# Kernel tuning notes

Hardware: AMD Instinct MI355X
Metric: run time of the kernel (lower is better)

## Reference

```python
import jax, jax.numpy as jnp
import numpy as np

N_MOLS, N_CONFS_PER, A = 64, 10, 40
N_CONFS = N_MOLS * N_CONFS_PER   # 640
N_ATOMS = N_CONFS * A            # 25600
N_EDGES = 409600
D, F, NG, L = 256, 256, 32, 4    # n_atom_basis, n_filters, n_gaussians, n_convolutions
MOL_BASIS = 512
CUTOFF = 5.0
LOG2 = float(np.log(2.0))


def ssp(x):
    # shifted softplus, the SchNet nonlinearity
    return jax.nn.softplus(x) - LOG2


def setup_inputs() -> dict:
    key = jax.random.key(0)
    ks = jax.random.split(key, 20)
    z = jax.random.randint(ks[0], (N_ATOMS,), 1, 100)          # atomic numbers (0 is padding)
    xyz = jax.random.normal(ks[1], (N_ATOMS, 3)) * 2.0
    # neighbor list: pairs of atoms within the same conformer block
    conf = jax.random.randint(ks[2], (N_EDGES,), 0, N_CONFS)
    i = conf * A + jax.random.randint(ks[3], (N_EDGES,), 0, A)
    j = conf * A + jax.random.randint(ks[4], (N_EDGES,), 0, A)
    nbr_list = jnp.stack([i, j], axis=1)
    # statistical boltzmann weights, normalized within each molecule
    w = jax.random.uniform(ks[5], (N_MOLS, N_CONFS_PER))
    boltz_weights = (w / w.sum(axis=1, keepdims=True)).reshape(-1)

    def glorot(k, shape):
        fan = shape[-2] + shape[-1]
        return jax.random.normal(k, shape) * np.sqrt(2.0 / fan)

    emb = (jax.random.normal(ks[6], (100, D)) * 0.1).at[0].set(0.0)  # padding_idx=0
    H = (D + MOL_BASIS) // 2  # 384
    params = dict(
        We1=glorot(ks[7], (L, NG, NG)), be1=jnp.zeros((L, NG)),
        We2=glorot(ks[8], (L, NG, F)),  be2=jnp.zeros((L, F)),
        Wn=glorot(ks[9], (L, D, F)),    bn=jnp.zeros((L, F)),
        Wu1=glorot(ks[10], (L, F, D)),  bu1=jnp.zeros((L, D)),
        Wu2=glorot(ks[11], (L, D, D)),  bu2=jnp.zeros((L, D)),
        Wm1=glorot(ks[12], (D, H)),            bm1=jnp.zeros((H,)),
        Wm2=glorot(ks[13], (H, MOL_BASIS)),    bm2=jnp.zeros((MOL_BASIS,)),
        Wr1=glorot(ks[14], (MOL_BASIS, MOL_BASIS // 2)), br1=jnp.zeros((MOL_BASIS // 2,)),
        Wr2=glorot(ks[15], (MOL_BASIS // 2, 1)),         br2=jnp.zeros((1,)),
    )
    return dict(z=z, xyz=xyz, nbr_list=nbr_list, boltz_weights=boltz_weights, emb=emb, **params)


def reference(z, xyz, nbr_list, boltz_weights, emb,
              We1, be1, We2, be2, Wn, bn, Wu1, bu1, Wu2, bu2,
              Wm1, bm1, Wm2, bm2, Wr1, br1, Wr2, br2):
    a0, a1 = nbr_list[:, 0], nbr_list[:, 1]
    # pair distances -> gaussian smearing (fixed, non-trainable) [E, NG]
    d = jnp.sqrt(jnp.sum((xyz[a0] - xyz[a1]) ** 2, axis=1))
    offsets = jnp.linspace(0.0, CUTOFF, NG)
    width = offsets[1] - offsets[0]
    e_g = jnp.exp(-0.5 * ((d[:, None] - offsets[None, :]) / width) ** 2)

    r = emb[z]  # [N, D] atom embeddings
    for l in range(L):
        # edge filter network: Dense -> ssp -> Dense,  [E, F]
        ef = ssp(e_g @ We1[l] + be1[l]) @ We2[l] + be2[l]
        # node filter [N, F]
        rn = r @ Wn[l] + bn[l]
        # symmetric gather-multiply-scatter (undirected neighbor list)
        agg = jax.ops.segment_sum(rn[a1] * ef, a0, num_segments=N_ATOMS)
        agg = agg + jax.ops.segment_sum(rn[a0] * ef, a1, num_segments=N_ATOMS)
        # update network with residual
        r = r + (ssp(agg @ Wu1[l] + bu1[l]) @ Wu2[l] + bu2[l])

    # sum-pool atoms into conformer fingerprints [C, D]
    conf_fp = r.reshape(N_CONFS, A, D).sum(axis=1)
    # mol_fp_nn -> [C, MOL_BASIS]
    mol_conf_fp = ssp(conf_fp @ Wm1 + bm1) @ Wm2 + bm2
    # boltzmann 'multiply': weight each conformer fp and sum per molecule
    mol_fp = (mol_conf_fp * boltz_weights[:, None]).reshape(N_MOLS, N_CONFS_PER, MOL_BASIS).sum(axis=1)
    # readout head (classifier -> sigmoid)
    out = jax.nn.sigmoid(ssp(mol_fp @ Wr1 + br1) @ Wr2 + br2)  # [N_MOLS, 1]
    return out
```

## Files before the change

kernel.cpp:

```cpp
#include <hip/hip_runtime.h>
#include <hip/hip_bf16.h>

#define N_MOLS      64
#define N_CONFS_PER 10
#define A_ATOMS     40
#define N_CONFS     640
#define N_ATOMS     25600
#define N_EDGES     409600
#define D           256
#define NG          32
#define NLAYERS     4
#define MOLB        512
#define H_MOL       384
#define EDGE_CAP    1024
#define EB          32
#define NBMAX       32
#define SHBP        36
#define SEFP        260
#define SBH         256
#define TPB         512

typedef __attribute__((ext_vector_type(8))) short bshort8;
typedef __attribute__((ext_vector_type(4))) float f32x4;

#define SWZ(row, hw) (((row) << 8) + ((hw) ^ (((row) & 7) << 3)))

__device__ __forceinline__ float sspf(float x) {
    return fmaxf(x, 0.f) + __logf(1.f + __expf(-fabsf(x))) - 0.69314718055994531f;
}
__device__ __forceinline__ float b2f(short s) {
    union { unsigned u; float f; } u;
    u.u = ((unsigned)(unsigned short)s) << 16;
    return u.f;
}
__device__ __forceinline__ short f2bf(float x) {
    return (short)(unsigned short)((__float_as_uint(x) + 0x8000u) >> 16);
}
__device__ __forceinline__ unsigned pkbf(float lo_e, float hi_e) {
    return __builtin_amdgcn_perm(__float_as_uint(hi_e) + 0x8000u,
                                 __float_as_uint(lo_e) + 0x8000u, 0x07060302u);
}

__global__ __launch_bounds__(256) void k_prep(const float* __restrict__ Wn,
                                              const float* __restrict__ Wu1,
                                              const float* __restrict__ Wu2,
                                              __hip_bfloat16* __restrict__ WT) {
    int idx = blockIdx.x * 256 + threadIdx.x;
    int k = idx & 255;
    int n = (idx >> 8) & 255;
    int l = (idx >> 16) & 3;
    int mat = idx >> 18;
    const float* src = (mat == 0) ? Wn : (mat == 1) ? Wu1 : Wu2;
    WT[idx] = __float2bfloat16(src[((size_t)l * 256 + k) * 256 + n]);
}

__global__ __launch_bounds__(256) void k_prep2(const float* __restrict__ We2,
                                               const float* __restrict__ We1,
                                               __hip_bfloat16* __restrict__ WT2,
                                               __hip_bfloat16* __restrict__ We1T) {
    int idx = blockIdx.x * 256 + threadIdx.x;
    if (idx < 32768) {
        int k = idx & 31;
        int n = (idx >> 5) & 255;
        int l = idx >> 13;
        WT2[idx] = __float2bfloat16(We2[((size_t)l * 32 + k) * 256 + n]);
    } else {
        int j = idx - 32768;
        int m = j & 31;
        int t = (j >> 5) & 31;
        int l = j >> 10;
        We1T[j] = __float2bfloat16(We1[((size_t)l * 32 + m) * 32 + t]);
    }
}

__global__ __launch_bounds__(256) void k_scatter(const int* __restrict__ nbr,
                                                 unsigned* __restrict__ cursors,
                                                 unsigned* __restrict__ esort) {
    int e = blockIdx.x * 256 + threadIdx.x;
    if (e >= N_EDGES) return;
    int a0 = nbr[2 * e], a1 = nbr[2 * e + 1];
    int conf = a0 / A_ATOMS;
    int a0l = a0 - conf * A_ATOMS;
    int a1l = a1 - conf * A_ATOMS;
    unsigned r = atomicAdd(&cursors[conf], 1u);
    if (r < EDGE_CAP) esort[conf * EDGE_CAP + r] = (unsigned)((a0l << 6) | a1l);
}

__device__ __forceinline__ void mfma_dense8b(const short* __restrict__ src,
                                             const __hip_bfloat16* __restrict__ WT,
                                             f32x4 acc[3][2], int lane, int wv) {
    const int r = lane & 15, g = lane >> 4;
#pragma unroll
    for (int mt = 0; mt < 3; ++mt)
#pragma unroll
        for (int j = 0; j < 2; ++j) acc[mt][j] = (f32x4){0.f, 0.f, 0.f, 0.f};
#pragma unroll 2
    for (int kt = 0; kt < 8; ++kt) {
        const int ko = kt * 32 + g * 8;
        bshort8 a0 = *(const bshort8*)&src[SWZ(0 * 16 + r, ko)];
        bshort8 a1 = *(const bshort8*)&src[SWZ(1 * 16 + r, ko)];
        bshort8 a2 = *(const bshort8*)&src[SWZ(2 * 16 + r, ko)];
#pragma unroll
        for (int j = 0; j < 2; ++j) {
            const int nt = wv * 2 + j;
            bshort8 b = *(const bshort8*)&WT[(nt * 16 + r) * 256 + ko];
            acc[0][j] = __builtin_amdgcn_mfma_f32_16x16x32_bf16(a0, b, acc[0][j], 0, 0, 0);
            acc[1][j] = __builtin_amdgcn_mfma_f32_16x16x32_bf16(a1, b, acc[1][j], 0, 0, 0);
            acc[2][j] = __builtin_amdgcn_mfma_f32_16x16x32_bf16(a2, b, acc[2][j], 0, 0, 0);
        }
    }
}

template <int MODE>
__device__ __forceinline__ void mfma_wb8b(const f32x4 acc[3][2], short* __restrict__ dst16,
                                          const float* __restrict__ bias, int lane, int wv) {
    const int cc = lane & 15, g = lane >> 4;
    const int cr = g * 4;
#pragma unroll
    for (int j = 0; j < 2; ++j) {
        const int col = (wv * 2 + j) * 16 + cc;
        const float bv = bias[col];
#pragma unroll
        for (int mt = 0; mt < 3; ++mt) {
            if (mt == 2 && g >= 2) continue;
#pragma unroll
            for (int reg = 0; reg < 4; ++reg) {
                const int row = mt * 16 + cr + reg;
                float v = acc[mt][j][reg] + bv;
                if (MODE == 1) v = sspf(v);
                dst16[SWZ(row, col)] = f2bf(v);
            }
        }
    }
}

__global__ __launch_bounds__(TPB, 4) void k_main(
    const int* __restrict__ z, const float* __restrict__ xyz,
    const float* __restrict__ emb,
    const float* __restrict__ be1, const float* __restrict__ be2,
    const float* __restrict__ bn,
    const float* __restrict__ bu1, const float* __restrict__ bu2,
    const __hip_bfloat16* __restrict__ WT,
    const __hip_bfloat16* __restrict__ WT2,
    const __hip_bfloat16* __restrict__ We1T,
    const unsigned* __restrict__ cursors, const unsigned* __restrict__ esort,
    float* __restrict__ conf_fp)
{
    __shared__ short sRb[48 * SBH];
    __shared__ short sBb[48 * SBH];
    __shared__ __align__(16) char uEFbuf[EB * SEFP * 2];
    __shared__ __align__(16) char sHbBuf[2 * EB * SHBP * 2];
    __shared__ float sDall[EDGE_CAP];
    __shared__ unsigned short sCsr[2 * EDGE_CAP];
    __shared__ unsigned short sWin[A_ATOMS * (NBMAX + 1)];
    __shared__ int sPtr[A_ATOMS + 1];

    short* sEFs = (short*)uEFbuf;
    float* colsum = (float*)uEFbuf;
    float (*sXYZ)[3] = (float(*)[3])uEFbuf;
    int* sZ   = (int*)(uEFbuf + 480);
    int* sDeg = (int*)(uEFbuf + 640);
    short (*sHb)[EB * SHBP] = (short(*)[EB * SHBP])sHbBuf;
    unsigned* sEdge = (unsigned*)sHbBuf;

    const int tid  = threadIdx.x;
    const int lane = tid & 63;
    const int wv   = tid >> 6;
    const int c4   = lane << 2;
    const int conf = blockIdx.x;
    const int fr = lane & 15, fg = lane >> 4, g8 = (lane >> 4) << 3;
    const int mtx = wv & 1;
    const int ttx = (wv >> 1) & 1;

    if (tid < A_ATOMS) {
        int ga = conf * A_ATOMS + tid;
        sZ[tid] = z[ga];
        sXYZ[tid][0] = xyz[ga * 3 + 0];
        sXYZ[tid][1] = xyz[ga * 3 + 1];
        sXYZ[tid][2] = xyz[ga * 3 + 2];
        sDeg[tid] = 0;
    }
    for (int i = tid; i < 8 * SBH; i += TPB) {
        sRb[40 * SBH + i] = 0;
        sBb[40 * SBH + i] = 0;
    }
    __syncthreads();
    float embsum = 0.f;
    {
        const int c = tid & 255, q = tid >> 8;
        for (int aa = q; aa < A_ATOMS; aa += 2) {
            float v = emb[sZ[aa] * D + c];
            embsum += v;
            sRb[SWZ(aa, c)] = f2bf(v);
        }
    }
    int cnt = (int)cursors[conf];
    if (cnt > EDGE_CAP) cnt = EDGE_CAP;
    const unsigned* eptr = esort + conf * EDGE_CAP;
    for (int i = tid; i < cnt; i += TPB) {
        unsigned pe = eptr[i];
        sEdge[i] = pe;
        int a0l = (pe >> 6) & 63, a1l = pe & 63;
        float dx = sXYZ[a0l][0] - sXYZ[a1l][0];
        float dy = sXYZ[a0l][1] - sXYZ[a1l][1];
        float dz = sXYZ[a0l][2] - sXYZ[a1l][2];
        sDall[i] = sqrtf(dx * dx + dy * dy + dz * dz) * (31.0f / 5.0f);
        atomicAdd(&sDeg[a0l], 1);
        atomicAdd(&sDeg[a1l], 1);
    }
    for (int i = cnt + tid; i < EDGE_CAP; i += TPB) sDall[i] = 0.f;
    __syncthreads();
    if (tid == 0) {
        int s = 0;
        for (int a = 0; a < A_ATOMS; ++a) { sPtr[a] = s; s += sDeg[a]; }
        sPtr[A_ATOMS] = s;
    }
    __syncthreads();
    const int NB = (cnt + EB - 1) / EB;
    if (tid < A_ATOMS) {
        const int ps = sPtr[tid];
        int pos = ps;
        for (int i = 0; i < cnt; ++i) {
            unsigned pe = sEdge[i];
            int a0l = (pe >> 6) & 63, a1l = pe & 63;
            if (a0l == tid) sCsr[pos++] = (unsigned short)((a1l << 10) | i);
            if (a1l == tid) sCsr[pos++] = (unsigned short)((a0l << 10) | i);
        }
        int p = ps;
        for (int b = 0; b <= NB; ++b) {
            const int lim = b * EB;
            while (p < pos && (int)(sCsr[p] & 1023) < lim) ++p;
            sWin[tid * (NBMAX + 1) + b] = (unsigned short)p;
        }
    }

    float csum[2] = {0.f, 0.f};

    for (int l = 0; l < NLAYERS; ++l) {
        __syncthreads();
        {
            f32x4 acc[3][2];
            mfma_dense8b(sRb, WT + ((size_t)(0 * 4 + l) << 16), acc, lane, wv);
            mfma_wb8b<0>(acc, sBb, bn + l * D, lane, wv);
        }
        __syncthreads();
        float4 agg[5];
#pragma unroll
        for (int k = 0; k < 5; ++k) agg[k] = make_float4(0.f, 0.f, 0.f, 0.f);
        {
            const bshort8 bf0 = *(const bshort8*)&WT2[(size_t)l * 8192 + ((2 * wv + 0) * 16 + fr) * 32 + g8];
            const bshort8 bf1 = *(const bshort8*)&WT2[(size_t)l * 8192 + ((2 * wv + 1) * 16 + fr) * 32 + g8];
            const float bb0 = be2[l * D + (2 * wv + 0) * 16 + fr];
            const float bb1 = be2[l * D + (2 * wv + 1) * 16 + fr];
            const bshort8 bfX = *(const bshort8*)&We1T[(size_t)l * 1024 + (ttx * 16 + fr) * 32 + g8];
            const float bbX = be1[l * NG + ttx * 16 + fr];

            if (wv < 4 && NB > 0) {
                const float dd = sDall[mtx * 16 + fr];
                union { bshort8 v; unsigned u[4]; } ua;
#pragma unroll
                for (int j = 0; j < 4; ++j) {
                    const float u0 = dd - (float)(g8 + 2 * j + 0);
                    const float u1 = dd - (float)(g8 + 2 * j + 1);
                    ua.u[j] = pkbf(__expf(-0.5f * u0 * u0), __expf(-0.5f * u1 * u1));
                }
                f32x4 c = (f32x4){0.f, 0.f, 0.f, 0.f};
                c = __builtin_amdgcn_mfma_f32_16x16x32_bf16(ua.v, bfX, c, 0, 0, 0);
#pragma unroll
                for (int reg = 0; reg < 4; ++reg) {
                    const int erow = mtx * 16 + fg * 4 + reg;
                    sHb[0][erow * SHBP + ttx * 16 + fr] = f2bf(sspf(c[reg] + bbX));
                }
            }
            __syncthreads();
            for (int b = 0; b < NB; ++b) {
                const int base = b * EB;
                {
                    const short* __restrict__ hb = sHb[b & 1];
#pragma unroll
                    for (int mt = 0; mt < 2; ++mt) {
                        union { bshort8 v; short4 s[2]; } af;
                        af.s[0] = *(const short4*)&hb[(mt * 16 + fr) * SHBP + g8];
                        af.s[1] = *(const short4*)&hb[(mt * 16 + fr) * SHBP + g8 + 4];
                        f32x4 c0 = (f32x4){0.f, 0.f, 0.f, 0.f};
                        c0 = __builtin_amdgcn_mfma_f32_16x16x32_bf16(af.v, bf0, c0, 0, 0, 0);
                        f32x4 c1 = (f32x4){0.f, 0.f, 0.f, 0.f};
                        c1 = __builtin_amdgcn_mfma_f32_16x16x32_bf16(af.v, bf1, c1, 0, 0, 0);
#pragma unroll
                        for (int reg = 0; reg < 4; ++reg) {
                            const int erow = mt * 16 + fg * 4 + reg;
                            sEFs[erow * SEFP + (2 * wv + 0) * 16 + fr] = f2bf(c0[reg] + bb0);
                            sEFs[erow * SEFP + (2 * wv + 1) * 16 + fr] = f2bf(c1[reg] + bb1);
                        }
                    }
                }
                if (wv < 4 && b + 1 < NB) {
                    short* __restrict__ hb = sHb[(b + 1) & 1];
                    const float dd = sDall[(b + 1) * EB + mtx * 16 + fr];
                    union { bshort8 v; unsigned u[4]; } ua;
#pragma unroll
                    for (int j = 0; j < 4; ++j) {
                        const float u0 = dd - (float)(g8 + 2 * j + 0);
                        const float u1 = dd - (float)(g8 + 2 * j + 1);
                        ua.u[j] = pkbf(__expf(-0.5f * u0 * u0), __expf(-0.5f * u1 * u1));
                    }
                    f32x4 c = (f32x4){0.f, 0.f, 0.f, 0.f};
                    c = __builtin_amdgcn_mfma_f32_16x16x32_bf16(ua.v, bfX, c, 0, 0, 0);
#pragma unroll
                    for (int reg = 0; reg < 4; ++reg) {
                        const int erow = mtx * 16 + fg * 4 + reg;
                        hb[erow * SHBP + ttx * 16 + fr] = f2bf(sspf(c[reg] + bbX));
                    }
                }
                __syncthreads();
#pragma unroll
                for (int k = 0; k < 5; ++k) {
                    const int row = wv * 5 + k;
                    const int st = (int)sWin[row * (NBMAX + 1) + b];
                    const int en = (int)sWin[row * (NBMAX + 1) + b + 1];
                    for (int i = st; i < en; ++i) {
                        const int ent = (int)sCsr[i];
                        const int e = ent & 1023, src = ent >> 10;
                        const short4 f4 = *(const short4*)&sEFs[(e - base) * SEFP + c4];
                        const short4 r4 = *(const short4*)&sBb[SWZ(src, c4)];
                        agg[k].x = fmaf(b2f(f4.x), b2f(r4.x), agg[k].x);
                        agg[k].y = fmaf(b2f(f4.y), b2f(r4.y), agg[k].y);
                        agg[k].z = fmaf(b2f(f4.z), b2f(r4.z), agg[k].z);
                        agg[k].w = fmaf(b2f(f4.w), b2f(r4.w), agg[k].w);
                    }
                }
                __syncthreads();
            }
        }
#pragma unroll
        for (int k = 0; k < 5; ++k) {
            uint2 p;
            p.x = pkbf(agg[k].x, agg[k].y);
            p.y = pkbf(agg[k].z, agg[k].w);
            *(uint2*)&sBb[SWZ(wv * 5 + k, c4)] = p;
        }
        __syncthreads();
        {
            f32x4 acc[3][2];
            mfma_dense8b(sBb, WT + ((size_t)(1 * 4 + l) << 16), acc, lane, wv);
            __syncthreads();
            mfma_wb8b<1>(acc, sBb, bu1 + l * D, lane, wv);
        }
        __syncthreads();
        {
            f32x4 acc[3][2];
            mfma_dense8b(sBb, WT + ((size_t)(2 * 4 + l) << 16), acc, lane, wv);
            const int cc = lane & 15, g = lane >> 4, cr = g * 4;
#pragma unroll
            for (int j = 0; j < 2; ++j) {
                const int col = (wv * 2 + j) * 16 + cc;
                const float bv = bu2[l * D + col];
#pragma unroll
                for (int mt = 0; mt < 3; ++mt) {
                    if (mt == 2 && g >= 2) continue;
#pragma unroll
                    for (int reg = 0; reg < 4; ++reg) {
                        const int row = mt * 16 + cr + reg;
                        float v = acc[mt][j][reg] + bv;
                        csum[j] += v;
                        const int idx = SWZ(row, col);
                        sRb[idx] = f2bf(b2f(sRb[idx]) + v);
                    }
                }
            }
        }
    }
    __syncthreads();
    if (tid < D) colsum[tid] = 0.f;
    __syncthreads();
    {
        const int cc = lane & 15;
#pragma unroll
        for (int j = 0; j < 2; ++j)
            atomicAdd(&colsum[(wv * 2 + j) * 16 + cc], csum[j]);
        atomicAdd(&colsum[tid & 255], embsum);
    }
    __syncthreads();
    if (tid < D) conf_fp[conf * D + tid] = colsum[tid];
}

__global__ __launch_bounds__(512) void k_mol(
    const float* __restrict__ conf_fp,
    const float* __restrict__ Wm1, const float* __restrict__ bm1,
    const float* __restrict__ Wm2, const float* __restrict__ bm2,
    const float* __restrict__ boltz, float* __restrict__ mol_fp)
{
    __shared__ float cf[D];
    __shared__ float t[H_MOL];
    const int conf = blockIdx.x;
    const int tid = threadIdx.x;
    if (tid < D) cf[tid] = conf_fp[conf * D + tid];
    __syncthreads();
    if (tid < H_MOL) {
        float s = bm1[tid];
        for (int k = 0; k < D; k += 4) {
            const float4 v = *(const float4*)&cf[k];
            s = fmaf(v.x, Wm1[(k + 0) * H_MOL + tid], s);
            s = fmaf(v.y, Wm1[(k + 1) * H_MOL + tid], s);
            s = fmaf(v.z, Wm1[(k + 2) * H_MOL + tid], s);
            s = fmaf(v.w, Wm1[(k + 3) * H_MOL + tid], s);
        }
        t[tid] = sspf(s);
    }
    __syncthreads();
    {
        const int m = tid;
        float s = bm2[m];
        for (int h = 0; h < H_MOL; h += 4) {
            const float4 v = *(const float4*)&t[h];
            s = fmaf(v.x, Wm2[(h + 0) * MOLB + m], s);
            s = fmaf(v.y, Wm2[(h + 1) * MOLB + m], s);
            s = fmaf(v.z, Wm2[(h + 2) * MOLB + m], s);
            s = fmaf(v.w, Wm2[(h + 3) * MOLB + m], s);
        }
        atomicAdd(&mol_fp[(conf / N_CONFS_PER) * MOLB + m], s * boltz[conf]);
    }
}

__global__ __launch_bounds__(256) void k_final(
    const float* __restrict__ mol_fp,
    const float* __restrict__ Wr1, const float* __restrict__ br1,
    const float* __restrict__ Wr2, const float* __restrict__ br2,
    float* __restrict__ out)
{
    __shared__ float mf[MOLB];
    __shared__ float t2[D];
    __shared__ float red[4];
    const int mol = blockIdx.x, tid = threadIdx.x;
    mf[tid]       = mol_fp[mol * MOLB + tid];
    mf[tid + 256] = mol_fp[mol * MOLB + tid + 256];
    __syncthreads();
    {
        float s = br1[tid];
        for (int k = 0; k < MOLB; k += 4) {
            const float4 v = *(const float4*)&mf[k];
            s = fmaf(v.x, Wr1[(k + 0) * D + tid], s);
            s = fmaf(v.y, Wr1[(k + 1) * D + tid], s);
            s = fmaf(v.z, Wr1[(k + 2) * D + tid], s);
            s = fmaf(v.w, Wr1[(k + 3) * D + tid], s);
        }
        t2[tid] = sspf(s);
    }
    __syncthreads();
    float p = t2[tid] * Wr2[tid];
#pragma unroll
    for (int o = 32; o > 0; o >>= 1) p += __shfl_down(p, o);
    if ((tid & 63) == 0) red[tid >> 6] = p;
    __syncthreads();
    if (tid == 0) {
        float logit = red[0] + red[1] + red[2] + red[3] + br2[0];
        out[mol] = 1.f / (1.f + expf(-logit));
    }
}

extern "C" void kernel_launch(void* const* d_in, const int* in_sizes, int n_in,
                              void* d_out, int out_size, void* d_ws, size_t ws_size,
                              hipStream_t stream)
{
    const int*   z     = (const int*)d_in[0];
    const float* xyz   = (const float*)d_in[1];
    const int*   nbr   = (const int*)d_in[2];
    const float* boltz = (const float*)d_in[3];
    const float* emb   = (const float*)d_in[4];
    const float* We1   = (const float*)d_in[5];
    const float* be1   = (const float*)d_in[6];
    const float* We2   = (const float*)d_in[7];
    const float* be2   = (const float*)d_in[8];
    const float* Wn    = (const float*)d_in[9];
    const float* bn    = (const float*)d_in[10];
    const float* Wu1   = (const float*)d_in[11];
    const float* bu1   = (const float*)d_in[12];
    const float* Wu2   = (const float*)d_in[13];
    const float* bu2   = (const float*)d_in[14];
    const float* Wm1   = (const float*)d_in[15];
    const float* bm1   = (const float*)d_in[16];
    const float* Wm2   = (const float*)d_in[17];
    const float* bm2   = (const float*)d_in[18];
    const float* Wr1   = (const float*)d_in[19];
    const float* br1   = (const float*)d_in[20];
    const float* Wr2   = (const float*)d_in[21];
    const float* br2   = (const float*)d_in[22];

    char* ws = (char*)d_ws;
    unsigned* cursors        = (unsigned*)ws;
    float*    mol_fp         = (float*)(ws + 2560);
    unsigned* esort          = (unsigned*)(ws + 133632);
    float*    conf_fp        = (float*)(ws + 2755072);
    __hip_bfloat16* WT       = (__hip_bfloat16*)(ws + 3410432);
    __hip_bfloat16* WT2      = (__hip_bfloat16*)(ws + 4983296);
    __hip_bfloat16* We1T     = (__hip_bfloat16*)(ws + 5048832);

    hipMemsetAsync(cursors, 0, 2560 + 131072, stream);
    k_prep<<<3072, 256, 0, stream>>>(Wn, Wu1, Wu2, WT);
    k_prep2<<<144, 256, 0, stream>>>(We2, We1, WT2, We1T);
    k_scatter<<<(N_EDGES + 255) / 256, 256, 0, stream>>>(nbr, cursors, esort);
    k_main<<<N_CONFS, TPB, 0, stream>>>(z, xyz, emb, be1, be2, bn,
                                        bu1, bu2, WT, WT2, We1T, cursors, esort, conf_fp);
    k_mol<<<N_CONFS, 512, 0, stream>>>(conf_fp, Wm1, bm1, Wm2, bm2, boltz, mol_fp);
    k_final<<<N_MOLS, 256, 0, stream>>>(mol_fp, Wr1, br1, Wr2, br2, (float*)d_out);
}
```

Baseline: 855.8 us.

## Merge prep kernels into one launch and fuse mol MLP into main kernel

Combines the three preprocessing kernels (weight transposes and edge bucketing) into a single launch partitioned by block index, and folds the per-conformer molecular MLP and Boltzmann-weighted accumulation into the tail of the main kernel, reading the conformer fingerprint straight from shared memory. This removes two kernel launches and the conf_fp round trip through global memory. In exchange the main kernel carries extra code and register pressure in its epilogue, which could hurt occupancy. The 384-float MLP scratch now shares the edge-filter buffer.

```diff
diff --git a/kernel.cpp b/kernel.cpp
--- a/kernel.cpp
+++ b/kernel.cpp
@@ -41,49 +41,50 @@
                                  __float_as_uint(lo_e) + 0x8000u, 0x07060302u);
 }
 
-__global__ __launch_bounds__(256) void k_prep(const float* __restrict__ Wn,
-                                              const float* __restrict__ Wu1,
-                                              const float* __restrict__ Wu2,
-                                              __hip_bfloat16* __restrict__ WT) {
-    int idx = blockIdx.x * 256 + threadIdx.x;
-    int k = idx & 255;
-    int n = (idx >> 8) & 255;
-    int l = (idx >> 16) & 3;
-    int mat = idx >> 18;
-    const float* src = (mat == 0) ? Wn : (mat == 1) ? Wu1 : Wu2;
-    WT[idx] = __float2bfloat16(src[((size_t)l * 256 + k) * 256 + n]);
-}
-
-__global__ __launch_bounds__(256) void k_prep2(const float* __restrict__ We2,
-                                               const float* __restrict__ We1,
-                                               __hip_bfloat16* __restrict__ WT2,
-                                               __hip_bfloat16* __restrict__ We1T) {
-    int idx = blockIdx.x * 256 + threadIdx.x;
-    if (idx < 32768) {
-        int k = idx & 31;
-        int n = (idx >> 5) & 255;
-        int l = idx >> 13;
-        WT2[idx] = __float2bfloat16(We2[((size_t)l * 32 + k) * 256 + n]);
+#define PREP_WT_BLOCKS   3072
+#define PREP_W2_BLOCKS   144
+#define PREP_SC_BLOCKS   1600
+__global__ __launch_bounds__(256) void k_prep_all(
+    const float* __restrict__ Wn, const float* __restrict__ Wu1,
+    const float* __restrict__ Wu2, const float* __restrict__ We2,
+    const float* __restrict__ We1, const int* __restrict__ nbr,
+    __hip_bfloat16* __restrict__ WT, __hip_bfloat16* __restrict__ WT2,
+    __hip_bfloat16* __restrict__ We1T,
+    unsigned* __restrict__ cursors, unsigned* __restrict__ esort)
+{
+    const int bid = blockIdx.x;
+    if (bid < PREP_WT_BLOCKS) {
+        int idx = bid * 256 + threadIdx.x;
+        int k = idx & 255;
+        int n = (idx >> 8) & 255;
+        int l = (idx >> 16) & 3;
+        int mat = idx >> 18;
+        const float* src = (mat == 0) ? Wn : (mat == 1) ? Wu1 : Wu2;
+        WT[idx] = __float2bfloat16(src[((size_t)l * 256 + k) * 256 + n]);
+    } else if (bid < PREP_WT_BLOCKS + PREP_W2_BLOCKS) {
+        int idx = (bid - PREP_WT_BLOCKS) * 256 + threadIdx.x;
+        if (idx < 32768) {
+            int k = idx & 31;
+            int n = (idx >> 5) & 255;
+            int l = idx >> 13;
+            WT2[idx] = __float2bfloat16(We2[((size_t)l * 32 + k) * 256 + n]);
+        } else {
+            int j = idx - 32768;
+            int m = j & 31;
+            int t = (j >> 5) & 31;
+            int l = j >> 10;
+            We1T[j] = __float2bfloat16(We1[((size_t)l * 32 + m) * 32 + t]);
+        }
     } else {
-        int j = idx - 32768;
-        int m = j & 31;
-        int t = (j >> 5) & 31;
-        int l = j >> 10;
-        We1T[j] = __float2bfloat16(We1[((size_t)l * 32 + m) * 32 + t]);
-    }
-}
-
-__global__ __launch_bounds__(256) void k_scatter(const int* __restrict__ nbr,
-                                                 unsigned* __restrict__ cursors,
-                                                 unsigned* __restrict__ esort) {
-    int e = blockIdx.x * 256 + threadIdx.x;
-    if (e >= N_EDGES) return;
-    int a0 = nbr[2 * e], a1 = nbr[2 * e + 1];
-    int conf = a0 / A_ATOMS;
-    int a0l = a0 - conf * A_ATOMS;
-    int a1l = a1 - conf * A_ATOMS;
-    unsigned r = atomicAdd(&cursors[conf], 1u);
-    if (r < EDGE_CAP) esort[conf * EDGE_CAP + r] = (unsigned)((a0l << 6) | a1l);
+        int e = (bid - PREP_WT_BLOCKS - PREP_W2_BLOCKS) * 256 + threadIdx.x;
+        if (e >= N_EDGES) return;
+        int a0 = nbr[2 * e], a1 = nbr[2 * e + 1];
+        int conf = a0 / A_ATOMS;
+        int a0l = a0 - conf * A_ATOMS;
+        int a1l = a1 - conf * A_ATOMS;
+        unsigned r = atomicAdd(&cursors[conf], 1u);
+        if (r < EDGE_CAP) esort[conf * EDGE_CAP + r] = (unsigned)((a0l << 6) | a1l);
+    }
 }
 
 __device__ __forceinline__ void mfma_dense8b(const short* __restrict__ src,
@@ -144,7 +145,9 @@
     const __hip_bfloat16* __restrict__ WT2,
     const __hip_bfloat16* __restrict__ We1T,
     const unsigned* __restrict__ cursors, const unsigned* __restrict__ esort,
-    float* __restrict__ conf_fp)
+    const float* __restrict__ Wm1, const float* __restrict__ bm1,
+    const float* __restrict__ Wm2, const float* __restrict__ bm2,
+    const float* __restrict__ boltz, float* __restrict__ mol_fp)
 {
     __shared__ short sRb[48 * SBH];
     __shared__ short sBb[48 * SBH];
@@ -157,6 +160,7 @@
 
     short* sEFs = (short*)uEFbuf;
     float* colsum = (float*)uEFbuf;
+    float* t1 = (float*)(uEFbuf + 1024);
     float (*sXYZ)[3] = (float(*)[3])uEFbuf;
     int* sZ   = (int*)(uEFbuf + 480);
     int* sDeg = (int*)(uEFbuf + 640);
@@ -381,44 +385,28 @@
         atomicAdd(&colsum[tid & 255], embsum);
     }
     __syncthreads();
-    if (tid < D) conf_fp[conf * D + tid] = colsum[tid];
-}
-
-__global__ __launch_bounds__(512) void k_mol(
-    const float* __restrict__ conf_fp,
-    const float* __restrict__ Wm1, const float* __restrict__ bm1,
-    const float* __restrict__ Wm2, const float* __restrict__ bm2,
-    const float* __restrict__ boltz, float* __restrict__ mol_fp)
-{
-    __shared__ float cf[D];
-    __shared__ float t[H_MOL];
-    const int conf = blockIdx.x;
-    const int tid = threadIdx.x;
-    if (tid < D) cf[tid] = conf_fp[conf * D + tid];
-    __syncthreads();
     if (tid < H_MOL) {
         float s = bm1[tid];
         for (int k = 0; k < D; k += 4) {
-            const float4 v = *(const float4*)&cf[k];
+            const float4 v = *(const float4*)&colsum[k];
             s = fmaf(v.x, Wm1[(k + 0) * H_MOL + tid], s);
             s = fmaf(v.y, Wm1[(k + 1) * H_MOL + tid], s);
             s = fmaf(v.z, Wm1[(k + 2) * H_MOL + tid], s);
             s = fmaf(v.w, Wm1[(k + 3) * H_MOL + tid], s);
         }
-        t[tid] = sspf(s);
+        t1[tid] = sspf(s);
     }
     __syncthreads();
     {
-        const int m = tid;
-        float s = bm2[m];
+        float s = bm2[tid];
         for (int h = 0; h < H_MOL; h += 4) {
-            const float4 v = *(const float4*)&t[h];
-            s = fmaf(v.x, Wm2[(h + 0) * MOLB + m], s);
-            s = fmaf(v.y, Wm2[(h + 1) * MOLB + m], s);
-            s = fmaf(v.z, Wm2[(h + 2) * MOLB + m], s);
-            s = fmaf(v.w, Wm2[(h + 3) * MOLB + m], s);
-        }
-        atomicAdd(&mol_fp[(conf / N_CONFS_PER) * MOLB + m], s * boltz[conf]);
+            const float4 v = *(const float4*)&t1[h];
+            s = fmaf(v.x, Wm2[(h + 0) * MOLB + tid], s);
+            s = fmaf(v.y, Wm2[(h + 1) * MOLB + tid], s);
+            s = fmaf(v.z, Wm2[(h + 2) * MOLB + tid], s);
+            s = fmaf(v.w, Wm2[(h + 3) * MOLB + tid], s);
+        }
+        atomicAdd(&mol_fp[(conf / N_CONFS_PER) * MOLB + tid], s * boltz[conf]);
     }
 }
 
@@ -490,17 +478,15 @@
     unsigned* cursors        = (unsigned*)ws;
     float*    mol_fp         = (float*)(ws + 2560);
     unsigned* esort          = (unsigned*)(ws + 133632);
-    float*    conf_fp        = (float*)(ws + 2755072);
     __hip_bfloat16* WT       = (__hip_bfloat16*)(ws + 3410432);
     __hip_bfloat16* WT2      = (__hip_bfloat16*)(ws + 4983296);
     __hip_bfloat16* We1T     = (__hip_bfloat16*)(ws + 5048832);
 
     hipMemsetAsync(cursors, 0, 2560 + 131072, stream);
-    k_prep<<<3072, 256, 0, stream>>>(Wn, Wu1, Wu2, WT);
-    k_prep2<<<144, 256, 0, stream>>>(We2, We1, WT2, We1T);
-    k_scatter<<<(N_EDGES + 255) / 256, 256, 0, stream>>>(nbr, cursors, esort);
+    k_prep_all<<<PREP_WT_BLOCKS + PREP_W2_BLOCKS + PREP_SC_BLOCKS, 256, 0, stream>>>(
+        Wn, Wu1, Wu2, We2, We1, nbr, WT, WT2, We1T, cursors, esort);
     k_main<<<N_CONFS, TPB, 0, stream>>>(z, xyz, emb, be1, be2, bn,
-                                        bu1, bu2, WT, WT2, We1T, cursors, esort, conf_fp);
-    k_mol<<<N_CONFS, 512, 0, stream>>>(conf_fp, Wm1, bm1, Wm2, bm2, boltz, mol_fp);
+                                        bu1, bu2, WT, WT2, We1T, cursors, esort,
+                                        Wm1, bm1, Wm2, bm2, boltz, mol_fp);
     k_final<<<N_MOLS, 256, 0, stream>>>(mol_fp, Wr1, br1, Wr2, br2, (float*)d_out);
 }
```

After: 844.6 us. No clear change (-1.3%).
